# Performance work log

Hardware: AMD Instinct MI355X
Metric: run time of the kernel (lower is better)

The kernel has to match this reference:

```python
import jax, jax.numpy as jnp
import numpy as np

SIGMA = 0.001
EPS_LOG = 1e-12
EPS_COS = 1e-8


def setup_inputs() -> dict:
    key = jax.random.key(0)
    k1, k2, k3, k4 = jax.random.split(key, 4)
    B, T, K, S, d = 32, 512, 8, 8, 300
    center_pos = jax.random.randint(k1, (B,), 0, T)
    query_token_ids = jax.random.randint(k2, (B, T), 0, 30000)
    center_sense_embeddings = jax.random.normal(k3, (B, K, d), dtype=jnp.float32)
    context_sense_embeddings = jax.random.normal(k4, (B, T - 1, S, d), dtype=jnp.float32)
    return {
        'center_pos': center_pos,
        'query_token_ids': query_token_ids,
        'center_sense_embeddings': center_sense_embeddings,
        'context_sense_embeddings': context_sense_embeddings,
    }


def reference(center_pos, query_token_ids, center_sense_embeddings, context_sense_embeddings):
    B, T = query_token_ids.shape
    d = center_sense_embeddings.shape[-1]
    # v: mean over senses of context tokens -> [B, C, d], C = T-1
    v = context_sense_embeddings.mean(axis=-2)
    # a: scaled dot between center senses and context vectors -> [B, C, K]
    a = jnp.einsum('bkd,bcd->bck', center_sense_embeddings, v) / jnp.sqrt(jnp.float32(d))
    # context positions: skip the center position (vectorized form of the per-batch loop)
    i = jnp.arange(T - 1)  # [C]
    ctx_pos = i[None, :] + (i[None, :] >= center_pos[:, None])  # [B, C]
    w = jnp.exp(-jnp.abs(ctx_pos - center_pos[:, None]).astype(jnp.float32) / SIGMA)
    logw = jnp.log(jnp.maximum(w, EPS_LOG))  # [B, C]
    alpha = jax.nn.softmax(a + logw[:, :, None], axis=1)  # softmax over context positions
    m = jnp.einsum('bck,bcd->bkd', alpha, v)  # [B, K, d]
    # cosine similarity along d (torch semantics: clamp each norm by eps)
    num = jnp.sum(center_sense_embeddings * m, axis=-1)
    n1 = jnp.linalg.norm(center_sense_embeddings, axis=-1)
    n2 = jnp.linalg.norm(m, axis=-1)
    s = num / (jnp.maximum(n1, EPS_COS) * jnp.maximum(n2, EPS_COS))  # [B, K]
    q = jax.nn.softmax(s, axis=-1)
    idx = jnp.argmax(q, axis=-1)  # [B]
    pooled = jnp.take_along_axis(center_sense_embeddings, idx[:, None, None], axis=1)[:, 0, :]  # [B, d]
    return pooled, q
```

## Files before the change

### kernel.cpp

```cpp
#include <hip/hip_runtime.h>

#define NB 32
#define NC 511
#define NK 8
#define NS 8
#define ND 300
#define ND4 75
#define CHUNK 16
#define NCHK 32
#define EPS_COS 1e-8f


__device__ __forceinline__ void f4add(float4& a, const float4& b) {
    a.x += b.x; a.y += b.y; a.z += b.z; a.w += b.w;
}
__device__ __forceinline__ void f4fma(float4& a, float s, const float4& b) {
    a.x += s * b.x; a.y += s * b.y; a.z += s * b.z; a.w += s * b.w;
}

__global__ __launch_bounds__(256) void k_fused(const float* __restrict__ ctx,
                                               const float* __restrict__ cen,
                                               float* __restrict__ part) {
    const int b     = blockIdx.x >> 5;
    const int chunk = blockIdx.x & 31;
    const int w     = threadIdx.x >> 6;
    const int lane  = threadIdx.x & 63;
    const int i0 = lane;
    const int i1 = lane + 64;
    const bool has1 = (i1 < ND4);

    const float4* cen4 = (const float4*)cen + (size_t)b * NK * ND4;

    float4 acc0[NK] = {};
    float4 acc1[NK] = {};

    const int cbase = chunk * CHUNK + w * 4;
#pragma unroll 1
    for (int u = 0; u < 4; ++u) {
        const int c = cbase + u;
        if (c >= NC) continue;

        const float4* ctx4 = (const float4*)ctx + (size_t)(b * NC + c) * NS * ND4;
        float4 s0 = make_float4(0.f, 0.f, 0.f, 0.f);
        float4 s1 = make_float4(0.f, 0.f, 0.f, 0.f);
#pragma unroll
        for (int sj = 0; sj < NS; ++sj) {
            float4 x = ctx4[sj * ND4 + i0];
            f4add(s0, x);
            if (has1) {
                float4 y = ctx4[sj * ND4 + i1];
                f4add(s1, y);
            }
        }
        const float inv = 0.125f;
        s0.x *= inv; s0.y *= inv; s0.z *= inv; s0.w *= inv;
        s1.x *= inv; s1.y *= inv; s1.z *= inv; s1.w *= inv;

        float pk[NK];
#pragma unroll
        for (int k = 0; k < NK; ++k) {
            float4 ca = cen4[k * ND4 + i0];
            float p = ca.x * s0.x + ca.y * s0.y + ca.z * s0.z + ca.w * s0.w;
            if (has1) {
                float4 cb = cen4[k * ND4 + i1];
                p += cb.x * s1.x + cb.y * s1.y + cb.z * s1.z + cb.w * s1.w;
            }
            pk[k] = p;
        }
#pragma unroll
        for (int off = 32; off; off >>= 1) {
#pragma unroll
            for (int k = 0; k < NK; ++k) pk[k] += __shfl_xor(pk[k], off);
        }
        const float scale = 0.057735026919f;
#pragma unroll
        for (int k = 0; k < NK; ++k) {
            float wk = __expf(pk[k] * scale);
            f4fma(acc0[k], wk, s0);
            if (has1) f4fma(acc1[k], wk, s1);
        }
    }

    __shared__ float lm[NK * ND];
    float4* lm4 = (float4*)lm;
    for (int wv = 0; wv < 4; ++wv) {
        if (w == wv) {
#pragma unroll
            for (int k = 0; k < NK; ++k) {
                if (wv == 0) {
                    lm4[k * ND4 + i0] = acc0[k];
                    if (has1) lm4[k * ND4 + i1] = acc1[k];
                } else {
                    float4 t4 = lm4[k * ND4 + i0];
                    f4add(t4, acc0[k]);
                    lm4[k * ND4 + i0] = t4;
                    if (has1) {
                        float4 u4 = lm4[k * ND4 + i1];
                        f4add(u4, acc1[k]);
                        lm4[k * ND4 + i1] = u4;
                    }
                }
            }
        }
        __syncthreads();
    }

    float4* pp4 = (float4*)(part + ((size_t)(b * NCHK + chunk)) * NK * ND);
    for (int idx = threadIdx.x; idx < NK * ND4; idx += 256)
        pp4[idx] = lm4[idx];
}

__global__ __launch_bounds__(256) void k_final(const float* __restrict__ part,
                                               const float* __restrict__ cen,
                                               float* __restrict__ out) {
    const int b = blockIdx.x;
    __shared__ float m[NK * ND];
    __shared__ float sred[NK];
    __shared__ int bidx;
    const int t = threadIdx.x;

    const float4* pb = (const float4*)(part + (size_t)b * NCHK * NK * ND);
    float4* m4 = (float4*)m;
    for (int idx = t; idx < NK * ND4; idx += 256) {
        float4 s = make_float4(0.f, 0.f, 0.f, 0.f);
#pragma unroll
        for (int ch = 0; ch < NCHK; ++ch)
            f4add(s, pb[(size_t)ch * NK * ND4 + idx]);
        m4[idx] = s;
    }
    __syncthreads();

    const int w = t >> 6, lane = t & 63;
#pragma unroll
    for (int kk = 0; kk < 2; ++kk) {
        const int k = w + kk * 4;
        const float* cp = cen + (size_t)(b * NK + k) * ND;
        const float* mp = m + k * ND;
        float num = 0.f, n1 = 0.f, n2 = 0.f;
        for (int dd = lane; dd < ND; dd += 64) {
            float cv = cp[dd], mv = mp[dd];
            num += cv * mv; n1 += cv * cv; n2 += mv * mv;
        }
#pragma unroll
        for (int off = 32; off; off >>= 1) {
            num += __shfl_down(num, off);
            n1  += __shfl_down(n1, off);
            n2  += __shfl_down(n2, off);
        }
        if (lane == 0) {
            float denom = fmaxf(sqrtf(n1), EPS_COS) * fmaxf(sqrtf(n2), EPS_COS);
            sred[k] = num / denom;
        }
    }
    __syncthreads();

    if (t == 0) {
        float mx = sred[0];
#pragma unroll
        for (int k = 1; k < NK; ++k) mx = fmaxf(mx, sred[k]);
        float e[NK], sum = 0.f;
#pragma unroll
        for (int k = 0; k < NK; ++k) { e[k] = __expf(sred[k] - mx); sum += e[k]; }
        float inv = 1.f / sum;
        int best = 0; float bv = sred[0];
#pragma unroll
        for (int k = 1; k < NK; ++k) if (sred[k] > bv) { bv = sred[k]; best = k; }
#pragma unroll
        for (int k = 0; k < NK; ++k)
            out[(size_t)NB * ND + b * NK + k] = e[k] * inv;
        bidx = best;
    }
    __syncthreads();

    const float* src = cen + (size_t)(b * NK + bidx) * ND;
    for (int idx = t; idx < ND; idx += 256)
        out[(size_t)b * ND + idx] = src[idx];
}

extern "C" void kernel_launch(void* const* d_in, const int* in_sizes, int n_in,
                              void* d_out, int out_size, void* d_ws, size_t ws_size,
                              hipStream_t stream) {
    const float* cen = (const float*)d_in[2];
    const float* ctx = (const float*)d_in[3];
    float* out = (float*)d_out;

    float* part = (float*)d_ws;

    k_fused<<<dim3(NB * NCHK), dim3(256), 0, stream>>>(ctx, cen, part);
    k_final<<<dim3(NB), dim3(256), 0, stream>>>(part, cen, out);
}
```

Measured before the change: 284.9 us.

## Assign one context row per wave, tree-reduce in LDS, split final reduction

The main kernel now uses 512-thread blocks where each of 8 waves handles a single context position, instead of 4 waves each looping over 4 positions. This gives more memory-level parallelism for streaming the large context tensor. The serialized per-wave LDS accumulation becomes a log-depth tree reduction, with wave 0 writing partials directly. The final reduction is split into a per-(batch,sense) kernel plus a small finalize kernel, which spreads the partial sums across 256 blocks but doubles the partial buffer (64 chunks) and adds a launch.

```diff
diff --git a/kernel.cpp b/kernel.cpp
--- a/kernel.cpp
+++ b/kernel.cpp
@@ -6,51 +6,39 @@
 #define NS 8
 #define ND 300
 #define ND4 75
-#define CHUNK 16
-#define NCHK 32
+#define NCHK 64
 #define EPS_COS 1e-8f
 
 
 __device__ __forceinline__ void f4add(float4& a, const float4& b) {
     a.x += b.x; a.y += b.y; a.z += b.z; a.w += b.w;
 }
-__device__ __forceinline__ void f4fma(float4& a, float s, const float4& b) {
-    a.x += s * b.x; a.y += s * b.y; a.z += s * b.z; a.w += s * b.w;
-}
 
-__global__ __launch_bounds__(256) void k_fused(const float* __restrict__ ctx,
-                                               const float* __restrict__ cen,
-                                               float* __restrict__ part) {
-    const int b     = blockIdx.x >> 5;
-    const int chunk = blockIdx.x & 31;
+__global__ __launch_bounds__(512) void k_main(const float* __restrict__ ctx,
+                                              const float* __restrict__ cen,
+                                              float* __restrict__ part) {
+    const int b     = blockIdx.x >> 6;
+    const int chunk = blockIdx.x & 63;
     const int w     = threadIdx.x >> 6;
     const int lane  = threadIdx.x & 63;
+    const int c     = chunk * 8 + w;
     const int i0 = lane;
     const int i1 = lane + 64;
     const bool has1 = (i1 < ND4);
 
-    const float4* cen4 = (const float4*)cen + (size_t)b * NK * ND4;
-
     float4 acc0[NK] = {};
     float4 acc1[NK] = {};
 
-    const int cbase = chunk * CHUNK + w * 4;
-#pragma unroll 1
-    for (int u = 0; u < 4; ++u) {
-        const int c = cbase + u;
-        if (c >= NC) continue;
+    if (c < NC) {
+        const float4* ctx4 = (const float4*)ctx + (size_t)(b * NC + c) * NS * ND4;
+        const float4* cen4 = (const float4*)cen + (size_t)b * NK * ND4;
 
-        const float4* ctx4 = (const float4*)ctx + (size_t)(b * NC + c) * NS * ND4;
         float4 s0 = make_float4(0.f, 0.f, 0.f, 0.f);
         float4 s1 = make_float4(0.f, 0.f, 0.f, 0.f);
 #pragma unroll
         for (int sj = 0; sj < NS; ++sj) {
-            float4 x = ctx4[sj * ND4 + i0];
-            f4add(s0, x);
-            if (has1) {
-                float4 y = ctx4[sj * ND4 + i1];
-                f4add(s1, y);
-            }
+            f4add(s0, ctx4[sj * ND4 + i0]);
+            if (has1) f4add(s1, ctx4[sj * ND4 + i1]);
         }
         const float inv = 0.125f;
         s0.x *= inv; s0.y *= inv; s0.z *= inv; s0.w *= inv;
@@ -76,102 +64,108 @@
 #pragma unroll
         for (int k = 0; k < NK; ++k) {
             float wk = __expf(pk[k] * scale);
-            f4fma(acc0[k], wk, s0);
-            if (has1) f4fma(acc1[k], wk, s1);
+            acc0[k].x = wk * s0.x; acc0[k].y = wk * s0.y;
+            acc0[k].z = wk * s0.z; acc0[k].w = wk * s0.w;
+            acc1[k].x = wk * s1.x; acc1[k].y = wk * s1.y;
+            acc1[k].z = wk * s1.z; acc1[k].w = wk * s1.w;
         }
     }
 
-    __shared__ float lm[NK * ND];
-    float4* lm4 = (float4*)lm;
-    for (int wv = 0; wv < 4; ++wv) {
-        if (w == wv) {
+    __shared__ float4 slab[4 * NK * ND4];
+#define SLAB_ST(slot) { float4* sp = slab + (slot) * NK * ND4;                  \
+    _Pragma("unroll") for (int k = 0; k < NK; ++k) {                            \
+        sp[k * ND4 + i0] = acc0[k];                                             \
+        if (has1) sp[k * ND4 + i1] = acc1[k]; } }
+#define SLAB_ADD(slot) { const float4* sp = slab + (slot) * NK * ND4;           \
+    _Pragma("unroll") for (int k = 0; k < NK; ++k) {                            \
+        f4add(acc0[k], sp[k * ND4 + i0]);                                       \
+        if (has1) f4add(acc1[k], sp[k * ND4 + i1]); } }
+
+    if (w >= 4) SLAB_ST(w - 4);
+    __syncthreads();
+    if (w < 4) SLAB_ADD(w);
+    __syncthreads();
+    if (w == 2 || w == 3) SLAB_ST(w - 2);
+    __syncthreads();
+    if (w < 2) SLAB_ADD(w);
+    __syncthreads();
+    if (w == 1) SLAB_ST(0);
+    __syncthreads();
+    if (w == 0) {
+        SLAB_ADD(0);
+        float4* pp = (float4*)part + (size_t)(b * NCHK + chunk) * NK * ND4;
 #pragma unroll
-            for (int k = 0; k < NK; ++k) {
-                if (wv == 0) {
-                    lm4[k * ND4 + i0] = acc0[k];
-                    if (has1) lm4[k * ND4 + i1] = acc1[k];
-                } else {
-                    float4 t4 = lm4[k * ND4 + i0];
-                    f4add(t4, acc0[k]);
-                    lm4[k * ND4 + i0] = t4;
-                    if (has1) {
-                        float4 u4 = lm4[k * ND4 + i1];
-                        f4add(u4, acc1[k]);
-                        lm4[k * ND4 + i1] = u4;
-                    }
-                }
-            }
+        for (int k = 0; k < NK; ++k) {
+            pp[k * ND4 + i0] = acc0[k];
+            if (has1) pp[k * ND4 + i1] = acc1[k];
         }
-        __syncthreads();
     }
-
-    float4* pp4 = (float4*)(part + ((size_t)(b * NCHK + chunk)) * NK * ND);
-    for (int idx = threadIdx.x; idx < NK * ND4; idx += 256)
-        pp4[idx] = lm4[idx];
+#undef SLAB_ST
+#undef SLAB_ADD
 }
 
-__global__ __launch_bounds__(256) void k_final(const float* __restrict__ part,
-                                               const float* __restrict__ cen,
-                                               float* __restrict__ out) {
+__global__ __launch_bounds__(320) void k_red(const float* __restrict__ part,
+                                             const float* __restrict__ cen,
+                                             float* __restrict__ sv) {
+    const int b = blockIdx.x >> 3;
+    const int k = blockIdx.x & 7;
+    const int t = threadIdx.x;
+    const int lane = t & 63, w = t >> 6;
+
+    float m = 0.f;
+    float cv = 0.f;
+    if (t < ND) {
+        const float* p = part + ((size_t)b * NCHK * NK + k) * ND + t;
+#pragma unroll 4
+        for (int ch = 0; ch < NCHK; ++ch)
+            m += p[(size_t)ch * NK * ND];
+        cv = cen[(size_t)(b * NK + k) * ND + t];
+    }
+    float num = cv * m, n1 = cv * cv, n2 = m * m;
+#pragma unroll
+    for (int off = 32; off; off >>= 1) {
+        num += __shfl_down(num, off);
+        n1  += __shfl_down(n1, off);
+        n2  += __shfl_down(n2, off);
+    }
+    __shared__ float red[5][3];
+    if (lane == 0) { red[w][0] = num; red[w][1] = n1; red[w][2] = n2; }
+    __syncthreads();
+    if (t == 0) {
+        float a0 = 0.f, a1 = 0.f, a2 = 0.f;
+#pragma unroll
+        for (int i = 0; i < 5; ++i) { a0 += red[i][0]; a1 += red[i][1]; a2 += red[i][2]; }
+        float denom = fmaxf(sqrtf(a1), EPS_COS) * fmaxf(sqrtf(a2), EPS_COS);
+        sv[b * NK + k] = a0 / denom;
+    }
+}
+
+__global__ __launch_bounds__(256) void k_fin(const float* __restrict__ sv,
+                                             const float* __restrict__ cen,
+                                             float* __restrict__ out) {
     const int b = blockIdx.x;
-    __shared__ float m[NK * ND];
-    __shared__ float sred[NK];
+    const int t = threadIdx.x;
     __shared__ int bidx;
-    const int t = threadIdx.x;
-
-    const float4* pb = (const float4*)(part + (size_t)b * NCHK * NK * ND);
-    float4* m4 = (float4*)m;
-    for (int idx = t; idx < NK * ND4; idx += 256) {
-        float4 s = make_float4(0.f, 0.f, 0.f, 0.f);
+    if (t == 0) {
+        float s[NK];
 #pragma unroll
-        for (int ch = 0; ch < NCHK; ++ch)
-            f4add(s, pb[(size_t)ch * NK * ND4 + idx]);
-        m4[idx] = s;
-    }
-    __syncthreads();
-
-    const int w = t >> 6, lane = t & 63;
+        for (int k = 0; k < NK; ++k) s[k] = sv[b * NK + k];
+        float mx = s[0];
 #pragma unroll
-    for (int kk = 0; kk < 2; ++kk) {
-        const int k = w + kk * 4;
-        const float* cp = cen + (size_t)(b * NK + k) * ND;
-        const float* mp = m + k * ND;
-        float num = 0.f, n1 = 0.f, n2 = 0.f;
-        for (int dd = lane; dd < ND; dd += 64) {
-            float cv = cp[dd], mv = mp[dd];
-            num += cv * mv; n1 += cv * cv; n2 += mv * mv;
-        }
-#pragma unroll
-        for (int off = 32; off; off >>= 1) {
-            num += __shfl_down(num, off);
-            n1  += __shfl_down(n1, off);
-            n2  += __shfl_down(n2, off);
-        }
-        if (lane == 0) {
-            float denom = fmaxf(sqrtf(n1), EPS_COS) * fmaxf(sqrtf(n2), EPS_COS);
-            sred[k] = num / denom;
-        }
-    }
-    __syncthreads();
-
-    if (t == 0) {
-        float mx = sred[0];
-#pragma unroll
-        for (int k = 1; k < NK; ++k) mx = fmaxf(mx, sred[k]);
+        for (int k = 1; k < NK; ++k) mx = fmaxf(mx, s[k]);
         float e[NK], sum = 0.f;
 #pragma unroll
-        for (int k = 0; k < NK; ++k) { e[k] = __expf(sred[k] - mx); sum += e[k]; }
+        for (int k = 0; k < NK; ++k) { e[k] = __expf(s[k] - mx); sum += e[k]; }
         float inv = 1.f / sum;
-        int best = 0; float bv = sred[0];
+        int best = 0; float bv = s[0];
 #pragma unroll
-        for (int k = 1; k < NK; ++k) if (sred[k] > bv) { bv = sred[k]; best = k; }
+        for (int k = 1; k < NK; ++k) if (s[k] > bv) { bv = s[k]; best = k; }
 #pragma unroll
         for (int k = 0; k < NK; ++k)
             out[(size_t)NB * ND + b * NK + k] = e[k] * inv;
         bidx = best;
     }
     __syncthreads();
-
     const float* src = cen + (size_t)(b * NK + bidx) * ND;
     for (int idx = t; idx < ND; idx += 256)
         out[(size_t)b * ND + idx] = src[idx];
@@ -185,7 +179,9 @@
     float* out = (float*)d_out;
 
     float* part = (float*)d_ws;
+    float* sv   = part + (size_t)NB * NCHK * NK * ND;
 
-    k_fused<<<dim3(NB * NCHK), dim3(256), 0, stream>>>(ctx, cen, part);
-    k_final<<<dim3(NB), dim3(256), 0, stream>>>(part, cen, out);
+    k_main<<<dim3(NB * NCHK), dim3(512), 0, stream>>>(ctx, cen, part);
+    k_red<<<dim3(NB * NK), dim3(320), 0, stream>>>(part, cen, sv);
+    k_fin<<<dim3(NB), dim3(256), 0, stream>>>(sv, cen, out);
 }
```

After: 274.8 us. 1.04x faster.
